# Performance work log

Measured on AMD Instinct MI355X. Metric: run time of the kernel, lower is better.

Reference implementation:

```python
import jax, jax.numpy as jnp
import numpy as np

D_MODEL = 1024
N_HEAD = 16
HEAD_DIM = D_MODEL // N_HEAD
LN_EPS = 1e-12


def setup_inputs() -> dict:
    key = jax.random.key(0)
    ks = jax.random.split(key, 9)
    B, S, D = 2, 2048, D_MODEL
    s = 1.0 / np.sqrt(D)
    return {
        "hidden_states": jax.random.normal(ks[0], (B, S, D), jnp.float32),
        "Wq": jax.random.normal(ks[1], (D, D), jnp.float32) * s,
        "bq": jnp.zeros((D,), jnp.float32),
        "Wk": jax.random.normal(ks[2], (D, D), jnp.float32) * s,
        "bk": jnp.zeros((D,), jnp.float32),
        "Wv": jax.random.normal(ks[3], (D, D), jnp.float32) * s,
        "bv": jnp.zeros((D,), jnp.float32),
        "Wo": jax.random.normal(ks[4], (D, D), jnp.float32) * s,
        "bo": jnp.zeros((D,), jnp.float32),
        "ln_gamma": jnp.ones((D,), jnp.float32),
        "ln_beta": jnp.zeros((D,), jnp.float32),
    }


def reference(hidden_states, Wq, bq, Wk, bk, Wv, bv, Wo, bo, ln_gamma, ln_beta):
    # BertAttention forward (eval mode: dropouts are identity).
    B, S, D = hidden_states.shape
    H, Dh = N_HEAD, HEAD_DIM

    def heads(x):  # [B,S,D] -> [B,H,S,Dh]
        return x.reshape(B, S, H, Dh).transpose(0, 2, 1, 3)

    q = heads(hidden_states @ Wq + bq)
    k = heads(hidden_states @ Wk + bk)
    v = heads(hidden_states @ Wv + bv)

    scores = jnp.einsum("bhsd,bhtd->bhst", q, k) / jnp.sqrt(jnp.float32(Dh))
    probs = jax.nn.softmax(scores, axis=-1)
    ctx = jnp.einsum("bhst,bhtd->bhsd", probs, v)
    ctx = ctx.transpose(0, 2, 1, 3).reshape(B, S, D)

    # BertSelfOutput: dense + residual + LayerNorm(eps=1e-12)
    h = ctx @ Wo + bo + hidden_states
    mu = jnp.mean(h, axis=-1, keepdims=True)
    var = jnp.mean(jnp.square(h - mu), axis=-1, keepdims=True)
    out = (h - mu) / jnp.sqrt(var + LN_EPS) * ln_gamma + ln_beta
    return out
```

## Files before the change

### kernel.cpp

```cpp
#include <hip/hip_runtime.h>
#include <hip/hip_bf16.h>

#define D_MODEL 1024
#define N_HEAD  16
#define HEAD_DIM 64
#define BATCH   2
#define SEQ     2048
#define M_ROWS  (BATCH * SEQ)

typedef unsigned short u16;
typedef unsigned int   u32;

typedef __attribute__((ext_vector_type(8))) short bfrag8;
typedef __attribute__((ext_vector_type(4))) float ffrag4;

__device__ __forceinline__ float bf2f(u16 u) {
    return __uint_as_float(((u32)u) << 16);
}
__device__ __forceinline__ u16 f2bf(float f) {
    u32 x = __float_as_uint(f);
    u32 r = (x + 0x7fffu + ((x >> 16) & 1u)) >> 16;
    return (u16)r;
}
__device__ __forceinline__ u32 pack_bf2_trunc(float lo, float hi) {
    return __builtin_amdgcn_perm(__float_as_uint(hi), __float_as_uint(lo),
                                 0x07060302u);
}
__device__ __forceinline__ float fast_exp2(float x) {
    float r;
    asm("v_exp_f32 %0, %1" : "=v"(r) : "v"(x));
    return r;
}

__device__ __forceinline__ void gl_lds16(const void* g, void* l) {
    __builtin_amdgcn_global_load_lds(
        (const __attribute__((address_space(1))) void*)g,
        (__attribute__((address_space(3))) void*)l, 16, 0, 0);
}

#define Q_PRESCALE 0.18033688011112042f

__device__ __forceinline__ int is_bf16(const u32* gb) {
    return gb[0] != 0x3F800000u;
}

__global__ __launch_bounds__(256) void prep_all(
    const void* w0, const void* w1, const void* w2, const void* w3,
    u16* t0, u16* t1, u16* t2, u16* t3,
    const void* v0, const void* v1, const void* v2, const void* v3,
    const void* v4, const void* v5, u16* __restrict__ vecs,
    const void* xsrc, u16* __restrict__ xdst, int xquads,
    const u32* __restrict__ gb)
{
    const int isbf = is_bf16(gb);
    const int tid = threadIdx.x;
    const int z = blockIdx.z;

    if (z < 4) {
        __shared__ u16 t[32][33];
        const void* srcs[4] = {w0, w1, w2, w3};
        u16* dsts[4] = {t0, t1, t2, t3};
        const void* src = srcs[z];
        u16* dst = dsts[z];
        const int bx = blockIdx.x * 32;
        const int by = blockIdx.y * 32;
        const int tx = tid & 31;
        const int ty = tid >> 5;
#pragma unroll
        for (int r = 0; r < 4; r++) {
            const int row = by + ty * 4 + r;
            u16 v;
            if (isbf) v = ((const u16*)src)[(size_t)row * D_MODEL + bx + tx];
            else      v = f2bf(((const float*)src)[(size_t)row * D_MODEL + bx + tx]);
            t[tx][ty * 4 + r] = v;
        }
        __syncthreads();
#pragma unroll
        for (int r = 0; r < 4; r++) {
            const int n = bx + ty * 4 + r;
            dst[(size_t)n * D_MODEL + by + tx] = t[ty * 4 + r][tx];
        }
        return;
    }

    const int id = blockIdx.y * 32 + blockIdx.x;
    if (id < 6) {
        const void* srcs[6] = {v0, v1, v2, v3, v4, v5};
        const void* src = srcs[id];
        u16* dst = vecs + (size_t)id * D_MODEL;
        if (isbf) {
            ((ushort4*)dst)[tid] = ((const ushort4*)src)[tid];
        } else {
            float4 v = ((const float4*)src)[tid];
            ushort4 o;
            o.x = f2bf(v.x); o.y = f2bf(v.y); o.z = f2bf(v.z); o.w = f2bf(v.w);
            ((ushort4*)dst)[tid] = o;
        }
        return;
    }
    if (isbf) return;
    const int nblk = 32 * 32 - 6;
    for (int i = (id - 6) * 256 + tid; i < xquads; i += nblk * 256) {
        float4 v = ((const float4*)xsrc)[i];
        ushort4 o;
        o.x = f2bf(v.x); o.y = f2bf(v.y); o.z = f2bf(v.z); o.w = f2bf(v.w);
        ((ushort4*)xdst)[i] = o;
    }
}

__global__ __launch_bounds__(256, 4) void qkv_mfma(
    const u16* __restrict__ Xraw, const u16* __restrict__ Xconv,
    const u32* __restrict__ gb,
    const u16* __restrict__ WqT, const u16* __restrict__ bq,
    const u16* __restrict__ WkT, const u16* __restrict__ bk,
    const u16* __restrict__ WvT, const u16* __restrict__ bv,
    u16* __restrict__ Qout, u16* __restrict__ Kout, u16* __restrict__ Vout)
{
    const u16* X = is_bf16(gb) ? Xraw : Xconv;

    __shared__ __align__(16) u16 SMEM[64 * 32 * 4];

    const int tid  = threadIdx.x;
    const int wave = tid >> 6;
    const int lane = tid & 63;
    const int quad = lane >> 4;
    const int l16  = lane & 15;
    const int m0 = blockIdx.y * 64;
    const int n0 = blockIdx.x * 64;
    const int wr = (wave >> 1) * 32;
    const int wc = (wave & 1) * 32;

    ffrag4 acc[3][2][2];
#pragma unroll
    for (int z = 0; z < 3; z++)
#pragma unroll
        for (int i = 0; i < 2; i++)
#pragma unroll
            for (int j = 0; j < 2; j++) acc[z][i][j] = (ffrag4){0.f, 0.f, 0.f, 0.f};

    const int srow  = wave * 16 + (lane >> 2);
    const int scolb = (lane & 3) * 16;
    const char* Ag  = (const char*)X   + (size_t)(m0 + srow) * (D_MODEL * 2) + scolb;
    const char* Bg0 = (const char*)WqT + (size_t)(n0 + srow) * (D_MODEL * 2) + scolb;
    const char* Bg1 = (const char*)WkT + (size_t)(n0 + srow) * (D_MODEL * 2) + scolb;
    const char* Bg2 = (const char*)WvT + (size_t)(n0 + srow) * (D_MODEL * 2) + scolb;
    char* lA  = (char*)SMEM + wave * 1024;
    char* lB0 = (char*)SMEM + 4096  + wave * 1024;
    char* lB1 = (char*)SMEM + 8192  + wave * 1024;
    char* lB2 = (char*)SMEM + 12288 + wave * 1024;

    for (int k0 = 0; k0 < D_MODEL; k0 += 32) {
        __syncthreads();
        gl_lds16(Ag  + (size_t)k0 * 2, lA);
        gl_lds16(Bg0 + (size_t)k0 * 2, lB0);
        gl_lds16(Bg1 + (size_t)k0 * 2, lB1);
        gl_lds16(Bg2 + (size_t)k0 * 2, lB2);
        __syncthreads();

        bfrag8 af[2];
#pragma unroll
        for (int mi = 0; mi < 2; mi++)
            af[mi] = *(const bfrag8*)((const char*)SMEM +
                       (wr + mi * 16 + l16) * 64 + quad * 16);
#pragma unroll
        for (int z = 0; z < 3; z++) {
            const char* Bz = (const char*)SMEM + 4096 + z * 4096;
            bfrag8 b0 = *(const bfrag8*)(Bz + (wc      + l16) * 64 + quad * 16);
            bfrag8 b1 = *(const bfrag8*)(Bz + (wc + 16 + l16) * 64 + quad * 16);
            acc[z][0][0] = __builtin_amdgcn_mfma_f32_16x16x32_bf16(af[0], b0, acc[z][0][0], 0, 0, 0);
            acc[z][0][1] = __builtin_amdgcn_mfma_f32_16x16x32_bf16(af[0], b1, acc[z][0][1], 0, 0, 0);
            acc[z][1][0] = __builtin_amdgcn_mfma_f32_16x16x32_bf16(af[1], b0, acc[z][1][0], 0, 0, 0);
            acc[z][1][1] = __builtin_amdgcn_mfma_f32_16x16x32_bf16(af[1], b1, acc[z][1][1], 0, 0, 0);
        }
    }

    __syncthreads();

    const int h = n0 >> 6;
    u16* T = SMEM + wave * (16 * 48);
#pragma unroll
    for (int z = 0; z < 2; z++) {
        const u16* bias = (z == 0) ? bq : bk;
        u16* Out        = (z == 0) ? Qout : Kout;
#pragma unroll
        for (int mi = 0; mi < 2; mi++) {
#pragma unroll
            for (int ni = 0; ni < 2; ni++) {
                const int col = ni * 16 + l16;
                const float bia = bf2f(bias[n0 + wc + col]);
#pragma unroll
                for (int r = 0; r < 4; r++) {
                    float v = acc[z][mi][ni][r] + bia;
                    if (z == 0) v *= Q_PRESCALE;
                    T[(quad * 4 + r) * 48 + col] = f2bf(v);
                }
            }
            asm volatile("s_waitcnt lgkmcnt(0)" ::: "memory");
            const int m = m0 + wr + mi * 16 + l16;
            const int b = m >> 11;
            const int s = m & 2047;
            u16* dst = Out + ((size_t)(b * N_HEAD + h) * SEQ + s) * HEAD_DIM
                           + wc + quad * 8;
            *(uint4*)dst = *(const uint4*)&T[l16 * 48 + quad * 8];
        }
    }

#pragma unroll
    for (int mi = 0; mi < 2; mi++) {
        const int mbase = m0 + wr + mi * 16 + quad * 4;
        const int b = mbase >> 11;
        const int s = mbase & 2047;
#pragma unroll
        for (int ni = 0; ni < 2; ni++) {
            const int n = n0 + wc + ni * 16 + l16;
            const float bia = bf2f(bv[n]);
            ushort4 o;
            o.x = f2bf(acc[2][mi][ni][0] + bia);
            o.y = f2bf(acc[2][mi][ni][1] + bia);
            o.z = f2bf(acc[2][mi][ni][2] + bia);
            o.w = f2bf(acc[2][mi][ni][3] + bia);
            *(ushort4*)&Vout[((size_t)(b * N_HEAD * HEAD_DIM + n)) * SEQ + s] = o;
        }
    }
}

__global__ __launch_bounds__(256, 2) void attn_mfma(
    const u16* __restrict__ Q, const u16* __restrict__ K,
    const u16* __restrict__ VT, u16* __restrict__ CTX)
{
    __shared__ __align__(16) u16 Ks[2][4096];
    __shared__ __align__(16) u16 Vs[2][4096];
    __shared__ __align__(16) u16 PQ[8192];

    const int tid  = threadIdx.x;
    const int wave = tid >> 6;
    const int lane = tid & 63;
    const int quad = lane >> 4;
    const int l16  = lane & 15;
    const int l7   = l16 & 7;

    const int b  = blockIdx.z;
    const int h  = blockIdx.y;
    const int q0 = blockIdx.x * 128;

    const size_t headoff = (size_t)(b * N_HEAD + h) * SEQ * HEAD_DIM;
    const u16* Qb  = Q  + headoff;
    const u16* Kb  = K  + headoff;
    const u16* VTb = VT + headoff;

    const int srow = tid >> 2;
    const int sc0  = (tid & 3) * 2;
    const int sd0  = srow * 64 + (((sc0    ) ^ (srow & 7)) << 3);
    const int sd1  = srow * 64 + (((sc0 + 1) ^ (srow & 7)) << 3);

    uint4 ka0 = *(const uint4*)&Kb[(size_t)srow * HEAD_DIM + sc0 * 8];
    uint4 ka1 = *(const uint4*)&Kb[(size_t)srow * HEAD_DIM + sc0 * 8 + 8];
    uint4 va0 = *(const uint4*)&VTb[(size_t)srow * SEQ + sc0 * 8];
    uint4 va1 = *(const uint4*)&VTb[(size_t)srow * SEQ + sc0 * 8 + 8];

    {
        const int qrow = tid >> 1;
        const int qcb  = (tid & 1) * 4;
#pragma unroll
        for (int i = 0; i < 4; i++) {
            uint4 v = *(const uint4*)&Qb[(size_t)(q0 + qrow) * HEAD_DIM + (qcb + i) * 8];
            *(uint4*)&PQ[qrow * 64 + (((qcb + i) ^ (qrow & 7)) << 3)] = v;
        }
    }
    __syncthreads();

    const int wq = wave * 32;
    bfrag8 qa[2][2];
#pragma unroll
    for (int g = 0; g < 2; g++)
#pragma unroll
        for (int ch = 0; ch < 2; ch++)
            qa[g][ch] = *(const bfrag8*)&PQ[(wq + g * 16 + l16) * 64 +
                                            (((ch * 4 + quad) ^ l7) << 3)];
    u16* Pw = &PQ[wave * 2048];

    ffrag4 oacc[2][4];
#pragma unroll
    for (int g = 0; g < 2; g++)
#pragma unroll
        for (int c = 0; c < 4; c++) oacc[g][c] = (ffrag4){0.f, 0.f, 0.f, 0.f};
    float lsum[2] = {0.f, 0.f};

    for (int t0 = 0; t0 < SEQ; t0 += 64) {
        const int buf = (t0 >> 6) & 1;
        u16* Kl = Ks[buf];
        u16* Vl = Vs[buf];
        *(uint4*)&Kl[sd0] = ka0;
        *(uint4*)&Kl[sd1] = ka1;
        *(uint4*)&Vl[sd0] = va0;
        *(uint4*)&Vl[sd1] = va1;
        __syncthreads();

        const int tn = (t0 + 64) & (SEQ - 1);
        ka0 = *(const uint4*)&Kb[(size_t)(tn + srow) * HEAD_DIM + sc0 * 8];
        ka1 = *(const uint4*)&Kb[(size_t)(tn + srow) * HEAD_DIM + sc0 * 8 + 8];
        va0 = *(const uint4*)&VTb[(size_t)srow * SEQ + tn + sc0 * 8];
        va1 = *(const uint4*)&VTb[(size_t)srow * SEQ + tn + sc0 * 8 + 8];

        ffrag4 st[4][2];
        __builtin_amdgcn_s_setprio(1);
#pragma unroll
        for (int c = 0; c < 4; c++) {
            const int kr = (c * 16 + l16) * 64;
            const bfrag8 kb0 = *(const bfrag8*)&Kl[kr + ((quad ^ l7) << 3)];
            const bfrag8 kb1 = *(const bfrag8*)&Kl[kr + (((4 + quad) ^ l7) << 3)];
#pragma unroll
            for (int g = 0; g < 2; g++) {
                ffrag4 a = (ffrag4){0.f, 0.f, 0.f, 0.f};
                a = __builtin_amdgcn_mfma_f32_16x16x32_bf16(kb0, qa[g][0], a, 0, 0, 0);
                a = __builtin_amdgcn_mfma_f32_16x16x32_bf16(kb1, qa[g][1], a, 0, 0, 0);
                st[c][g] = a;
            }
        }
        __builtin_amdgcn_s_setprio(0);

#pragma unroll
        for (int g = 0; g < 2; g++) {
            float part = 0.f;
#pragma unroll
            for (int c = 0; c < 4; c++) {
                const float e0 = fast_exp2(st[c][g][0]);
                const float e1 = fast_exp2(st[c][g][1]);
                const float e2 = fast_exp2(st[c][g][2]);
                const float e3 = fast_exp2(st[c][g][3]);
                part += (e0 + e1) + (e2 + e3);
                uint2 pk;
                pk.x = pack_bf2_trunc(e0, e1);
                pk.y = pack_bf2_trunc(e2, e3);
                const int chunk = 2 * c + (quad >> 1);
                *(uint2*)&Pw[(g * 16 + l16) * 64 + ((chunk ^ l7) << 3) +
                             (quad & 1) * 4] = pk;
            }
            part += __shfl_xor(part, 16);
            part += __shfl_xor(part, 32);
            lsum[g] += part;
        }

        asm volatile("s_waitcnt lgkmcnt(0)" ::: "memory");

        bfrag8 pa[2][2];
#pragma unroll
        for (int g = 0; g < 2; g++)
#pragma unroll
            for (int ch = 0; ch < 2; ch++)
                pa[g][ch] = *(const bfrag8*)&Pw[(g * 16 + l16) * 64 +
                                                (((ch * 4 + quad) ^ l7) << 3)];
        __builtin_amdgcn_s_setprio(1);
#pragma unroll
        for (int c = 0; c < 4; c++) {
            const int vr = (c * 16 + l16) * 64;
            const bfrag8 vb0 = *(const bfrag8*)&Vl[vr + ((quad ^ l7) << 3)];
            const bfrag8 vb1 = *(const bfrag8*)&Vl[vr + (((4 + quad) ^ l7) << 3)];
#pragma unroll
            for (int g = 0; g < 2; g++) {
                oacc[g][c] = __builtin_amdgcn_mfma_f32_16x16x32_bf16(pa[g][0], vb0, oacc[g][c], 0, 0, 0);
                oacc[g][c] = __builtin_amdgcn_mfma_f32_16x16x32_bf16(pa[g][1], vb1, oacc[g][c], 0, 0, 0);
            }
        }
        __builtin_amdgcn_s_setprio(0);
    }

#pragma unroll
    for (int g = 0; g < 2; g++) {
        float linv[4];
#pragma unroll
        for (int r = 0; r < 4; r++)
            linv[r] = 1.0f / __shfl(lsum[g], quad * 4 + r, 16);
#pragma unroll
        for (int c = 0; c < 4; c++) {
#pragma unroll
            for (int r = 0; r < 4; r++) {
                const int row = q0 + wq + g * 16 + quad * 4 + r;
                const int dh  = c * 16 + l16;
                CTX[(size_t)(b * SEQ + row) * D_MODEL + h * HEAD_DIM + dh] =
                    f2bf(oacc[g][c][r] * linv[r]);
            }
        }
    }
}

__global__ __launch_bounds__(256) void out_proj_mfma(
    const u16* __restrict__ CTX, const u16* __restrict__ WoT,
    const u16* __restrict__ bo, const u16* __restrict__ Xraw,
    const u16* __restrict__ Xconv, const u32* __restrict__ gb,
    u16* __restrict__ H)
{
    const u16* X = is_bf16(gb) ? Xraw : Xconv;
    __shared__ __align__(16) u16 SMEM[128 * 32 + 64 * 32];
    u16* As = SMEM;
    u16* Bs = SMEM + 128 * 32;

    const int tid  = threadIdx.x;
    const int wave = tid >> 6;
    const int lane = tid & 63;
    const int quad = lane >> 4;
    const int l16  = lane & 15;
    const int m0 = blockIdx.y * 128;
    const int n0 = blockIdx.x * 64;
    const int wr = (wave >> 1) * 64;
    const int wc = (wave & 1) * 32;

    ffrag4 acc[4][2];
#pragma unroll
    for (int i = 0; i < 4; i++)
#pragma unroll
        for (int j = 0; j < 2; j++) acc[i][j] = (ffrag4){0.f, 0.f, 0.f, 0.f};

    const int srowA = wave * 32 + (lane >> 2);
    const int srowB = wave * 16 + (lane >> 2);
    const int scolb = (lane & 3) * 16;
    const char* Ag = (const char*)CTX + (size_t)(m0 + srowA) * (D_MODEL * 2) + scolb;
    const char* Wg = (const char*)WoT + (size_t)(n0 + srowB) * (D_MODEL * 2) + scolb;
    char* lA = (char*)As + wave * 2048;
    char* lB = (char*)Bs + wave * 1024;
    const size_t rstep16 = (size_t)16 * (D_MODEL * 2);

    for (int k0 = 0; k0 < D_MODEL; k0 += 32) {
        __syncthreads();
        gl_lds16(Ag + (size_t)k0 * 2,           lA);
        gl_lds16(Ag + (size_t)k0 * 2 + rstep16, lA + 1024);
        gl_lds16(Wg + (size_t)k0 * 2,           lB);
        __syncthreads();

        bfrag8 af[4], bf[2];
#pragma unroll
        for (int mi = 0; mi < 4; mi++)
            af[mi] = *(const bfrag8*)((const char*)As + (wr + mi * 16 + l16) * 64 + quad * 16);
#pragma unroll
        for (int ni = 0; ni < 2; ni++)
            bf[ni] = *(const bfrag8*)((const char*)Bs + (wc + ni * 16 + l16) * 64 + quad * 16);
#pragma unroll
        for (int mi = 0; mi < 4; mi++)
#pragma unroll
            for (int ni = 0; ni < 2; ni++)
                acc[mi][ni] = __builtin_amdgcn_mfma_f32_16x16x32_bf16(
                    af[mi], bf[ni], acc[mi][ni], 0, 0, 0);
    }

    __syncthreads();

    float* T = (float*)SMEM + wave * (16 * 36);
#pragma unroll
    for (int mi = 0; mi < 4; mi++) {
#pragma unroll
        for (int ni = 0; ni < 2; ni++) {
            const int col = ni * 16 + l16;
#pragma unroll
            for (int r = 0; r < 4; r++)
                T[(quad * 4 + r) * 36 + col] = acc[mi][ni][r];
        }
        asm volatile("s_waitcnt lgkmcnt(0)" ::: "memory");
        const int m = m0 + wr + mi * 16 + l16;
        const int c = quad * 8;
        float4 v0 = *(const float4*)&T[l16 * 36 + c];
        float4 v1 = *(const float4*)&T[l16 * 36 + c + 4];
        const int n = n0 + wc + c;
        ushort4 b0 = *(const ushort4*)&bo[n];
        ushort4 b1 = *(const ushort4*)&bo[n + 4];
        ushort4 x0 = *(const ushort4*)&X[(size_t)m * D_MODEL + n];
        ushort4 x1 = *(const ushort4*)&X[(size_t)m * D_MODEL + n + 4];
        u16 o0 = f2bf(v0.x + bf2f(b0.x) + bf2f(x0.x));
        u16 o1 = f2bf(v0.y + bf2f(b0.y) + bf2f(x0.y));
        u16 o2 = f2bf(v0.z + bf2f(b0.z) + bf2f(x0.z));
        u16 o3 = f2bf(v0.w + bf2f(b0.w) + bf2f(x0.w));
        u16 o4 = f2bf(v1.x + bf2f(b1.x) + bf2f(x1.x));
        u16 o5 = f2bf(v1.y + bf2f(b1.y) + bf2f(x1.y));
        u16 o6 = f2bf(v1.z + bf2f(b1.z) + bf2f(x1.z));
        u16 o7 = f2bf(v1.w + bf2f(b1.w) + bf2f(x1.w));
        uint4 ov;
        ov.x = (u32)o0 | ((u32)o1 << 16);
        ov.y = (u32)o2 | ((u32)o3 << 16);
        ov.z = (u32)o4 | ((u32)o5 << 16);
        ov.w = (u32)o6 | ((u32)o7 << 16);
        *(uint4*)&H[(size_t)m * D_MODEL + n] = ov;
    }
}

__global__ __launch_bounds__(256) void ln_kernel(
    const u16* __restrict__ H, const u16* __restrict__ gamma,
    const u16* __restrict__ beta, void* __restrict__ out,
    const u32* __restrict__ gb)
{
    const int isbf = is_bf16(gb);
    const int row = blockIdx.x;
    const int tid = threadIdx.x;
    const u16* hr = H + (size_t)row * D_MODEL;

    ushort4 hv = *(const ushort4*)&hr[tid * 4];
    float v0 = bf2f(hv.x), v1 = bf2f(hv.y), v2 = bf2f(hv.z), v3 = bf2f(hv.w);
    float s  = (v0 + v1) + (v2 + v3);
    float ss = (v0 * v0 + v1 * v1) + (v2 * v2 + v3 * v3);

#pragma unroll
    for (int off = 1; off < 64; off <<= 1) {
        s  += __shfl_xor(s, off);
        ss += __shfl_xor(ss, off);
    }
    __shared__ float sbuf[4], ssbuf[4];
    const int w = tid >> 6;
    if ((tid & 63) == 0) { sbuf[w] = s; ssbuf[w] = ss; }
    __syncthreads();
    s  = sbuf[0] + sbuf[1] + sbuf[2] + sbuf[3];
    ss = ssbuf[0] + ssbuf[1] + ssbuf[2] + ssbuf[3];

    const float mu  = s * (1.f / D_MODEL);
    const float var = ss * (1.f / D_MODEL) - mu * mu;
    const float inv = rsqrtf(var + 1e-12f);

    const int n = tid * 4;
    ushort4 g4 = *(const ushort4*)&gamma[n];
    ushort4 b4 = *(const ushort4*)&beta[n];
    float o0 = (v0 - mu) * inv * bf2f(g4.x) + bf2f(b4.x);
    float o1 = (v1 - mu) * inv * bf2f(g4.y) + bf2f(b4.y);
    float o2 = (v2 - mu) * inv * bf2f(g4.z) + bf2f(b4.z);
    float o3 = (v3 - mu) * inv * bf2f(g4.w) + bf2f(b4.w);

    if (isbf) {
        ushort4 ov;
        ov.x = f2bf(o0); ov.y = f2bf(o1); ov.z = f2bf(o2); ov.w = f2bf(o3);
        *(ushort4*)&((u16*)out)[(size_t)row * D_MODEL + n] = ov;
    } else {
        *(float4*)&((float*)out)[(size_t)row * D_MODEL + n] =
            make_float4(o0, o1, o2, o3);
    }
}

extern "C" void kernel_launch(void* const* d_in, const int* in_sizes, int n_in,
                              void* d_out, int out_size, void* d_ws, size_t ws_size,
                              hipStream_t stream) {
    const size_t NTOK = (size_t)M_ROWS * D_MODEL;
    const size_t NW   = (size_t)D_MODEL * D_MODEL;
    const size_t NV   = D_MODEL;

    char* wp = (char*)d_ws;
    u16* Xc   = (u16*)wp;                 wp += NTOK * 2;
    u16* WqT  = (u16*)wp;                 wp += NW * 2;
    u16* WkT  = (u16*)wp;                 wp += NW * 2;
    u16* WvT  = (u16*)wp;                 wp += NW * 2;
    u16* WoT  = (u16*)wp;                 wp += NW * 2;
    u16* vecs = (u16*)wp;                 wp += 6 * NV * 2;
    u16* Q    = (u16*)wp;                 wp += NTOK * 2;
    u16* Kt   = (u16*)wp;                 wp += NTOK * 2;
    u16* Vt   = (u16*)wp;                 wp += NTOK * 2;
    u16* H    = Q;
    u16* CTX  = (u16*)d_out;

    u16* bqc = vecs + 0 * NV;
    u16* bkc = vecs + 1 * NV;
    u16* bvc = vecs + 2 * NV;
    u16* boc = vecs + 3 * NV;
    u16* gc  = vecs + 4 * NV;
    u16* bc  = vecs + 5 * NV;

    const u16* Xraw = (const u16*)d_in[0];
    const u32* gb   = (const u32*)d_in[9];

    prep_all<<<dim3(32, 32, 5), 256, 0, stream>>>(
        d_in[1], d_in[3], d_in[5], d_in[7], WqT, WkT, WvT, WoT,
        d_in[2], d_in[4], d_in[6], d_in[8], d_in[9], d_in[10], vecs,
        d_in[0], Xc, (int)(NTOK / 4), gb);

    qkv_mfma<<<dim3(D_MODEL / 64, M_ROWS / 64), 256, 0, stream>>>(
        Xraw, Xc, gb, WqT, bqc, WkT, bkc, WvT, bvc, Q, Kt, Vt);
    attn_mfma<<<dim3(SEQ / 128, N_HEAD, BATCH), 256, 0, stream>>>(Q, Kt, Vt, CTX);
    out_proj_mfma<<<dim3(D_MODEL / 64, M_ROWS / 128), 256, 0, stream>>>(
        CTX, WoT, boc, Xraw, Xc, gb, H);
    ln_kernel<<<M_ROWS, 256, 0, stream>>>(H, gc, bc, d_out, gb);
}
```

Measured before the change: 212.0 us.

## Double-buffer QKV GEMM with larger M tile, K=64 steps, and XOR-swizzled LDS

Restructures the fused QKV projection kernel to use a 128-row M tile, 64-wide K steps, and two LDS buffers so the next tile's global-to-LDS loads are issued while MFMAs consume the current one. Each wave now computes a 64x32 output per projection, raising MFMA work per LDS fragment load. LDS chunks are XOR-swizzled by row to cut bank conflicts on fragment reads. The cost is doubled accumulator registers and more LDS (occupancy bound lowered to 2), plus half as many blocks in the grid.

New measurement: 201.1 us. -5.2%, faster.

```diff
diff --git a/kernel.cpp b/kernel.cpp
--- a/kernel.cpp
+++ b/kernel.cpp
@@ -108,7 +108,7 @@
     }
 }
 
-__global__ __launch_bounds__(256, 4) void qkv_mfma(
+__global__ __launch_bounds__(256, 2) void qkv_mfma(
     const u16* __restrict__ Xraw, const u16* __restrict__ Xconv,
     const u32* __restrict__ gb,
     const u16* __restrict__ WqT, const u16* __restrict__ bq,
@@ -118,72 +118,92 @@
 {
     const u16* X = is_bf16(gb) ? Xraw : Xconv;
 
-    __shared__ __align__(16) u16 SMEM[64 * 32 * 4];
+    __shared__ __align__(16) u16 SMEM[2][20480];
 
     const int tid  = threadIdx.x;
     const int wave = tid >> 6;
     const int lane = tid & 63;
     const int quad = lane >> 4;
     const int l16  = lane & 15;
-    const int m0 = blockIdx.y * 64;
+    const int l7   = l16 & 7;
+    const int m0 = blockIdx.y * 128;
     const int n0 = blockIdx.x * 64;
-    const int wr = (wave >> 1) * 32;
+    const int wr = (wave >> 1) * 64;
     const int wc = (wave & 1) * 32;
 
-    ffrag4 acc[3][2][2];
+    ffrag4 acc[3][4][2];
 #pragma unroll
     for (int z = 0; z < 3; z++)
 #pragma unroll
-        for (int i = 0; i < 2; i++)
+        for (int i = 0; i < 4; i++)
 #pragma unroll
             for (int j = 0; j < 2; j++) acc[z][i][j] = (ffrag4){0.f, 0.f, 0.f, 0.f};
 
-    const int srow  = wave * 16 + (lane >> 2);
-    const int scolb = (lane & 3) * 16;
-    const char* Ag  = (const char*)X   + (size_t)(m0 + srow) * (D_MODEL * 2) + scolb;
-    const char* Bg0 = (const char*)WqT + (size_t)(n0 + srow) * (D_MODEL * 2) + scolb;
-    const char* Bg1 = (const char*)WkT + (size_t)(n0 + srow) * (D_MODEL * 2) + scolb;
-    const char* Bg2 = (const char*)WvT + (size_t)(n0 + srow) * (D_MODEL * 2) + scolb;
-    char* lA  = (char*)SMEM + wave * 1024;
-    char* lB0 = (char*)SMEM + 4096  + wave * 1024;
-    char* lB1 = (char*)SMEM + 8192  + wave * 1024;
-    char* lB2 = (char*)SMEM + 12288 + wave * 1024;
-
-    for (int k0 = 0; k0 < D_MODEL; k0 += 32) {
+    const int srow8 = lane >> 3;
+    const int scolb = ((lane & 7) ^ srow8) * 16;
+    const size_t rstep8 = (size_t)8 * (D_MODEL * 2);
+    const char* Ag  = (const char*)X   + (size_t)(m0 + wave * 32 + srow8) * (D_MODEL * 2) + scolb;
+    const char* Bg0 = (const char*)WqT + (size_t)(n0 + wave * 16 + srow8) * (D_MODEL * 2) + scolb;
+    const char* Bg1 = (const char*)WkT + (size_t)(n0 + wave * 16 + srow8) * (D_MODEL * 2) + scolb;
+    const char* Bg2 = (const char*)WvT + (size_t)(n0 + wave * 16 + srow8) * (D_MODEL * 2) + scolb;
+
+#define QKV_STAGE(bufp, kbyte)                                              \
+    {                                                                       \
+        char* Lb = (char*)SMEM[bufp];                                       \
+        _Pragma("unroll")                                                   \
+        for (int j = 0; j < 4; j++)                                         \
+            gl_lds16(Ag + (kbyte) + j * rstep8,                             \
+                     Lb + wave * 4096 + j * 1024);                          \
+        _Pragma("unroll")                                                   \
+        for (int j = 0; j < 2; j++) {                                       \
+            gl_lds16(Bg0 + (kbyte) + j * rstep8,                            \
+                     Lb + 16384 + wave * 2048 + j * 1024);                  \
+            gl_lds16(Bg1 + (kbyte) + j * rstep8,                            \
+                     Lb + 16384 + 8192 + wave * 2048 + j * 1024);           \
+            gl_lds16(Bg2 + (kbyte) + j * rstep8,                            \
+                     Lb + 16384 + 16384 + wave * 2048 + j * 1024);          \
+        }                                                                   \
+    }
+
+    QKV_STAGE(0, 0);
+    int cur = 0;
+    for (int k0 = 0; k0 < D_MODEL; k0 += 64) {
         __syncthreads();
-        gl_lds16(Ag  + (size_t)k0 * 2, lA);
-        gl_lds16(Bg0 + (size_t)k0 * 2, lB0);
-        gl_lds16(Bg1 + (size_t)k0 * 2, lB1);
-        gl_lds16(Bg2 + (size_t)k0 * 2, lB2);
-        __syncthreads();
-
-        bfrag8 af[2];
-#pragma unroll
-        for (int mi = 0; mi < 2; mi++)
-            af[mi] = *(const bfrag8*)((const char*)SMEM +
-                       (wr + mi * 16 + l16) * 64 + quad * 16);
-#pragma unroll
-        for (int z = 0; z < 3; z++) {
-            const char* Bz = (const char*)SMEM + 4096 + z * 4096;
-            bfrag8 b0 = *(const bfrag8*)(Bz + (wc      + l16) * 64 + quad * 16);
-            bfrag8 b1 = *(const bfrag8*)(Bz + (wc + 16 + l16) * 64 + quad * 16);
-            acc[z][0][0] = __builtin_amdgcn_mfma_f32_16x16x32_bf16(af[0], b0, acc[z][0][0], 0, 0, 0);
-            acc[z][0][1] = __builtin_amdgcn_mfma_f32_16x16x32_bf16(af[0], b1, acc[z][0][1], 0, 0, 0);
-            acc[z][1][0] = __builtin_amdgcn_mfma_f32_16x16x32_bf16(af[1], b0, acc[z][1][0], 0, 0, 0);
-            acc[z][1][1] = __builtin_amdgcn_mfma_f32_16x16x32_bf16(af[1], b1, acc[z][1][1], 0, 0, 0);
-        }
-    }
+        if (k0 + 64 < D_MODEL) QKV_STAGE(cur ^ 1, (size_t)(k0 + 64) * 2);
+        const char* Lb = (const char*)SMEM[cur];
+#pragma unroll
+        for (int kk = 0; kk < 2; kk++) {
+            const int chunk = ((kk * 4 + quad) ^ l7) * 16;
+            bfrag8 af[4];
+#pragma unroll
+            for (int mi = 0; mi < 4; mi++)
+                af[mi] = *(const bfrag8*)(Lb + (wr + mi * 16 + l16) * 128 + chunk);
+#pragma unroll
+            for (int z = 0; z < 3; z++) {
+                const char* Bz = Lb + 16384 + z * 8192;
+                bfrag8 b0 = *(const bfrag8*)(Bz + (wc + l16) * 128 + chunk);
+                bfrag8 b1 = *(const bfrag8*)(Bz + (wc + 16 + l16) * 128 + chunk);
+#pragma unroll
+                for (int mi = 0; mi < 4; mi++) {
+                    acc[z][mi][0] = __builtin_amdgcn_mfma_f32_16x16x32_bf16(af[mi], b0, acc[z][mi][0], 0, 0, 0);
+                    acc[z][mi][1] = __builtin_amdgcn_mfma_f32_16x16x32_bf16(af[mi], b1, acc[z][mi][1], 0, 0, 0);
+                }
+            }
+        }
+        cur ^= 1;
+    }
+#undef QKV_STAGE
 
     __syncthreads();
 
     const int h = n0 >> 6;
-    u16* T = SMEM + wave * (16 * 48);
+    u16* T = (u16*)SMEM[0] + wave * (16 * 48);
 #pragma unroll
     for (int z = 0; z < 2; z++) {
         const u16* bias = (z == 0) ? bq : bk;
         u16* Out        = (z == 0) ? Qout : Kout;
 #pragma unroll
-        for (int mi = 0; mi < 2; mi++) {
+        for (int mi = 0; mi < 4; mi++) {
 #pragma unroll
             for (int ni = 0; ni < 2; ni++) {
                 const int col = ni * 16 + l16;
@@ -206,7 +226,7 @@
     }
 
 #pragma unroll
-    for (int mi = 0; mi < 2; mi++) {
+    for (int mi = 0; mi < 4; mi++) {
         const int mbase = m0 + wr + mi * 16 + quad * 4;
         const int b = mbase >> 11;
         const int s = mbase & 2047;
@@ -565,7 +585,7 @@
         d_in[2], d_in[4], d_in[6], d_in[8], d_in[9], d_in[10], vecs,
         d_in[0], Xc, (int)(NTOK / 4), gb);
 
-    qkv_mfma<<<dim3(D_MODEL / 64, M_ROWS / 64), 256, 0, stream>>>(
+    qkv_mfma<<<dim3(D_MODEL / 64, M_ROWS / 128), 256, 0, stream>>>(
         Xraw, Xc, gb, WqT, bqc, WkT, bkc, WvT, bvc, Q, Kt, Vt);
     attn_mfma<<<dim3(SEQ / 128, N_HEAD, BATCH), 256, 0, stream>>>(Q, Kt, Vt, CTX);
     out_proj_mfma<<<dim3(D_MODEL / 64, M_ROWS / 128), 256, 0, stream>>>(
```
